# Kernel tuning notes

Measured on AMD Instinct MI355X. Metric: run time of the kernel, lower is better.

Reference implementation:

```python
import jax, jax.numpy as jnp
import numpy as np

# Model hyperparameters (from init_kwargs)
B, C, H, W = 4, 3, 224, 224
P = 16            # patch size
E = 768           # embed_dim
NH = 12           # num_heads
DH = E // NH      # head dim
L = 2             # num_layers
DFF = 4 * E
OUT = 1000
NP_ = (H // P) * (W // P)   # 196 patches
ALPHA, BETA, GAMMA = 0.5, 0.5, 1.0
EPS = 1e-8
LN_EPS = 1e-5


def _layernorm(x, w, b):
    mu = x.mean(-1, keepdims=True)
    var = ((x - mu) ** 2).mean(-1, keepdims=True)
    return (x - mu) * jax.lax.rsqrt(var + LN_EPS) * w + b


def _tversky_attn(x, ln_w, ln_b, w_qkv, b_qkv, w_o, b_o):
    # x: [B,S,E]
    h = _layernorm(x, ln_w, ln_b)
    qkv = h @ w_qkv + b_qkv                       # [B,S,3E]
    q, k, v = jnp.split(qkv, 3, axis=-1)
    def heads(t):
        return t.reshape(t.shape[0], t.shape[1], NH, DH).transpose(0, 2, 1, 3)  # [B,NH,S,DH]
    q, k, v = heads(q), heads(k), heads(v)
    # Tversky similarity on non-negative feature memberships
    qp = jax.nn.relu(q)
    kp = jax.nn.relu(k)
    qs = qp.sum(-1)                               # [B,NH,S]
    ks = kp.sum(-1)                               # [B,NH,S]
    # pairwise L1: sum_d |q_i - k_j|   (dominant intermediate [B,NH,S,S,DH])
    l1 = jnp.abs(qp[:, :, :, None, :] - kp[:, :, None, :, :]).sum(-1)  # [B,NH,S,S]
    qsum = qs[:, :, :, None]
    ksum = ks[:, :, None, :]
    inter = 0.5 * (qsum + ksum - l1)              # sum min(q,k)
    a_minus_b = 0.5 * (l1 + qsum - ksum)          # sum relu(q-k)
    b_minus_a = 0.5 * (l1 - qsum + ksum)          # sum relu(k-q)
    scores = GAMMA * inter / (inter + ALPHA * a_minus_b + BETA * b_minus_a + EPS)
    attn = jax.nn.softmax(scores, axis=-1)        # [B,NH,S,S]
    o = jnp.einsum('bhij,bhjd->bhid', attn, v)    # [B,NH,S,DH]
    o = o.transpose(0, 2, 1, 3).reshape(x.shape[0], x.shape[1], E)
    return o @ w_o + b_o


def _forward(x, conv_w, conv_b, pos_embed, cls_token,
             ln1_w, ln1_b, attn_w, attn_b, proj_w, proj_b,
             ln2_w, ln2_b, fc1_w, fc1_b, fc2_w, fc2_b,
             lnf_w, lnf_b, head_w, head_b):
    b = x.shape[0]
    # patch embed: stride==kernel conv == non-overlapping patch projection
    xp = x.reshape(b, C, H // P, P, W // P, P)
    tok = jnp.einsum('bchpwq,ecpq->bhwe', xp, conv_w).reshape(b, NP_, E) + conv_b
    tok = tok + pos_embed                         # [B,196,E]
    cls = jnp.broadcast_to(cls_token, (b, 1, E))
    h = jnp.concatenate([cls, tok], axis=1)       # [B,197,E]
    for i in range(L):
        h = h + _tversky_attn(h, ln1_w[i], ln1_b[i], attn_w[i], attn_b[i], proj_w[i], proj_b[i])
        m = _layernorm(h, ln2_w[i], ln2_b[i])
        m = jax.nn.gelu(m @ fc1_w[i] + fc1_b[i])
        h = h + m @ fc2_w[i] + fc2_b[i]
    h = _layernorm(h, lnf_w, lnf_b)
    return h[:, 0] @ head_w + head_b              # [B,OUT]


def setup_inputs() -> dict:
    key = jax.random.key(0)
    ks = jax.random.split(key, 24)
    n = lambda k, shp, s=0.02: jax.random.normal(k, shp, dtype=jnp.float32) * s
    return {
        'x': jax.random.normal(ks[0], (B, C, H, W), dtype=jnp.float32),
        'conv_w': n(ks[1], (E, C, P, P)),
        'conv_b': jnp.zeros((E,), jnp.float32),
        'pos_embed': n(ks[2], (1, NP_, E)),
        'cls_token': n(ks[3], (1, 1, E)),
        'ln1_w': jnp.ones((L, E), jnp.float32),
        'ln1_b': jnp.zeros((L, E), jnp.float32),
        'attn_w': n(ks[4], (L, E, 3 * E)),
        'attn_b': jnp.zeros((L, 3 * E), jnp.float32),
        'proj_w': n(ks[5], (L, E, E)),
        'proj_b': jnp.zeros((L, E), jnp.float32),
        'ln2_w': jnp.ones((L, E), jnp.float32),
        'ln2_b': jnp.zeros((L, E), jnp.float32),
        'fc1_w': n(ks[6], (L, E, DFF)),
        'fc1_b': jnp.zeros((L, DFF), jnp.float32),
        'fc2_w': n(ks[7], (L, DFF, E)),
        'fc2_b': jnp.zeros((L, E), jnp.float32),
        'lnf_w': jnp.ones((E,), jnp.float32),
        'lnf_b': jnp.zeros((E,), jnp.float32),
        'head_w': n(ks[8], (E, OUT)),
        'head_b': jnp.zeros((OUT,), jnp.float32),
    }


def reference(x, conv_w, conv_b, pos_embed, cls_token,
              ln1_w, ln1_b, attn_w, attn_b, proj_w, proj_b,
              ln2_w, ln2_b, fc1_w, fc1_b, fc2_w, fc2_b,
              lnf_w, lnf_b, head_w, head_b):
    return _forward(x, conv_w, conv_b, pos_embed, cls_token,
                    ln1_w, ln1_b, attn_w, attn_b, proj_w, proj_b,
                    ln2_w, ln2_b, fc1_w, fc1_b, fc2_w, fc2_b,
                    lnf_w, lnf_b, head_w, head_b)
```

## Files before the change

### kernel.cpp

```cpp
#include <hip/hip_runtime.h>
#include <hip/hip_bf16.h>
#include <math.h>

#define B_  4
#define E_  768
#define NH_ 12
#define DH_ 64
#define DFF_ 3072
#define OUT_ 1000
#define S_  197
#define ROWS_ 788
#define QH_P 12608
#define KGP  16384

typedef __bf16 bf16x8_t __attribute__((ext_vector_type(8)));
typedef float f32x4_t __attribute__((ext_vector_type(4)));
typedef _Float16 f16x2_t __attribute__((ext_vector_type(2)));

#define HAS_FDOT2 __has_builtin(__builtin_amdgcn_fdot2)

__device__ __forceinline__ float gelu_f(float x) {
    float x3 = x * x * x;
    return 0.5f * x * (1.0f + tanhf(0.7978845608028654f * (x + 0.044715f * x3)));
}
__device__ __forceinline__ ushort f_to_bf16bits(float f) {
    __hip_bfloat16 b = __float2bfloat16(f);
    return *(ushort*)&b;
}
__device__ __forceinline__ ushort f_to_f16bits(float f) {
    _Float16 h = (_Float16)f;
    return __builtin_bit_cast(ushort, h);
}
__device__ __forceinline__ f16x2_t u2h(uint u) { return __builtin_bit_cast(f16x2_t, u); }
__device__ __forceinline__ f16x2_t min2(f16x2_t a, f16x2_t b) {
    return __builtin_elementwise_min(a, b);
}

#define WT_CONV   0
#define WT_LBASE  589824
#define WT_LSTRIDE 7077888
#define WT_QKV    0
#define WT_PROJ   1769472
#define WT_FC1    2359296
#define WT_FC2    4718592
__global__ __launch_bounds__(256) void prep_all_kernel(const float* __restrict__ x,
                                                       __hip_bfloat16* __restrict__ aim,
                                                       const float* __restrict__ attn_w,
                                                       const float* __restrict__ proj_w,
                                                       const float* __restrict__ fc1_w,
                                                       const float* __restrict__ fc2_w,
                                                       const float* __restrict__ conv_w,
                                                       __hip_bfloat16* __restrict__ wt) {
    int bid = blockIdx.x;
    if (bid < 588) {
        int id = bid * 256 + threadIdx.x;
        int row = id / 192, k4 = (id - row * 192) * 4;
        int b = row / 196, pr = row - b * 196;
        int hp = pr / 14, wp = pr - hp * 14;
        int c = k4 >> 8, rem = k4 & 255, p = rem >> 4, q = rem & 15;
        float4 v = *(const float4*)&x[(((size_t)(b * 3 + c) * 224) + hp * 16 + p) * 224 + wp * 16 + q];
        ushort4 o = make_ushort4(f_to_bf16bits(v.x), f_to_bf16bits(v.y), f_to_bf16bits(v.z), f_to_bf16bits(v.w));
        *(ushort4*)((ushort*)aim + (size_t)row * 768 + k4) = o;
        return;
    }
    int id = bid - 588;
    if (id < 3456) {
        int l = id / 1728, r = id - l * 1728;
        const float* src;
        __hip_bfloat16* dst;
        int K, N, tile;
        size_t lbase = WT_LBASE + (size_t)l * WT_LSTRIDE;
        if (r < 432)       { src = attn_w + (size_t)l * E_ * 3 * E_; dst = wt + lbase + WT_QKV;  K = E_;   N = 3 * E_; tile = r; }
        else if (r < 576)  { src = proj_w + (size_t)l * E_ * E_;     dst = wt + lbase + WT_PROJ; K = E_;   N = E_;     tile = r - 432; }
        else if (r < 1152) { src = fc1_w + (size_t)l * E_ * DFF_;    dst = wt + lbase + WT_FC1;  K = E_;   N = DFF_;   tile = r - 576; }
        else               { src = fc2_w + (size_t)l * DFF_ * E_;    dst = wt + lbase + WT_FC2;  K = DFF_; N = E_;     tile = r - 1152; }
        int ntn = N >> 6;
        int kb = (tile / ntn) * 64, nb = (tile % ntn) * 64;
        int kq = (threadIdx.x & 15) * 4, nq = (threadIdx.x >> 4) * 4;
        const float* s0 = src + (size_t)(kb + kq) * N + nb + nq;
        float4 v0 = *(const float4*)(s0);
        float4 v1 = *(const float4*)(s0 + N);
        float4 v2 = *(const float4*)(s0 + 2 * N);
        float4 v3 = *(const float4*)(s0 + 3 * N);
        __hip_bfloat16* d0 = dst + (size_t)(nb + nq) * K + kb + kq;
        *(ushort4*)(d0)         = make_ushort4(f_to_bf16bits(v0.x), f_to_bf16bits(v1.x), f_to_bf16bits(v2.x), f_to_bf16bits(v3.x));
        *(ushort4*)(d0 + K)     = make_ushort4(f_to_bf16bits(v0.y), f_to_bf16bits(v1.y), f_to_bf16bits(v2.y), f_to_bf16bits(v3.y));
        *(ushort4*)(d0 + 2 * K) = make_ushort4(f_to_bf16bits(v0.z), f_to_bf16bits(v1.z), f_to_bf16bits(v2.z), f_to_bf16bits(v3.z));
        *(ushort4*)(d0 + 3 * K) = make_ushort4(f_to_bf16bits(v0.w), f_to_bf16bits(v1.w), f_to_bf16bits(v2.w), f_to_bf16bits(v3.w));
        return;
    }
    {
        int off = ((id - 3456) * 256 + threadIdx.x) * 4;
        float4 v = *(const float4*)&conv_w[off];
        ushort4 o = make_ushort4(f_to_bf16bits(v.x), f_to_bf16bits(v.y), f_to_bf16bits(v.z), f_to_bf16bits(v.w));
        *(ushort4*)((ushort*)wt + WT_CONV + off) = o;
    }
}

#define BK 64
#define AP 72
__global__ __launch_bounds__(256) void gemm_mfma_kernel(const __hip_bfloat16* __restrict__ A,
                                                        const __hip_bfloat16* __restrict__ WT,
                                                        const float* __restrict__ bias,
                                                        const float* __restrict__ res,
                                                        float* __restrict__ Cf,
                                                        __hip_bfloat16* __restrict__ Cb,
                                                        float* __restrict__ partbase,
                                                        int M, int N, int K, int act, int KS,
                                                        int res_pitch, int pn, int nofs) {
    __shared__ __align__(16) ushort Asb[2][64 * AP];
    __shared__ __align__(16) ushort Bsb[2][64 * AP];
    const int tid = threadIdx.x;
    const int wave = tid >> 6, lane = tid & 63;
    const int quad = lane >> 4, l15 = lane & 15;
    const int wm = wave >> 1, wn = wave & 1;
    const int m0 = blockIdx.y * 64, n0 = blockIdx.x * 64;

    const int Kc   = K / KS;
    const int kbeg = blockIdx.z * Kc;
    const int n_it = Kc / BK;

    f32x4_t acc[2][2] = {};

    const int c0r = tid >> 3,         c0o = (tid & 7) * 8;
    const int c1r = (tid + 256) >> 3, c1o = c0o;

    uint4 pa0, pa1, pb0, pb1;
    auto load_tile = [&](int kk) {
        pa0 = make_uint4(0, 0, 0, 0);
        pa1 = pa0;
        int gm = m0 + c0r;
        if (gm < M) pa0 = *(const uint4*)&A[(size_t)gm * K + kk + c0o];
        gm = m0 + c1r;
        if (gm < M) pa1 = *(const uint4*)&A[(size_t)gm * K + kk + c1o];
        pb0 = *(const uint4*)&WT[(size_t)(n0 + c0r) * K + kk + c0o];
        pb1 = *(const uint4*)&WT[(size_t)(n0 + c1r) * K + kk + c1o];
    };
    auto store_tile = [&](int buf) {
        *(uint4*)&Asb[buf][c0r * AP + c0o] = pa0;
        *(uint4*)&Asb[buf][c1r * AP + c1o] = pa1;
        *(uint4*)&Bsb[buf][c0r * AP + c0o] = pb0;
        *(uint4*)&Bsb[buf][c1r * AP + c1o] = pb1;
    };

    load_tile(kbeg);
    store_tile(0);
    if (n_it > 1) load_tile(kbeg + BK);
    __syncthreads();

    for (int it = 0; it < n_it; ++it) {
        const int cur = it & 1, nxt = cur ^ 1;
        if (it + 1 < n_it) {
            store_tile(nxt);
            if (it + 2 < n_it) load_tile(kbeg + (it + 2) * BK);
        }
        const ushort* As = Asb[cur];
        const ushort* Bs = Bsb[cur];
#pragma unroll
        for (int ks = 0; ks < BK; ks += 32) {
            bf16x8_t a0 = *(const bf16x8_t*)&As[(32 * wm + l15) * AP + ks + 8 * quad];
            bf16x8_t a1 = *(const bf16x8_t*)&As[(32 * wm + 16 + l15) * AP + ks + 8 * quad];
            bf16x8_t b0 = *(const bf16x8_t*)&Bs[(32 * wn + l15) * AP + ks + 8 * quad];
            bf16x8_t b1 = *(const bf16x8_t*)&Bs[(32 * wn + 16 + l15) * AP + ks + 8 * quad];
            acc[0][0] = __builtin_amdgcn_mfma_f32_16x16x32_bf16(a0, b0, acc[0][0], 0, 0, 0);
            acc[0][1] = __builtin_amdgcn_mfma_f32_16x16x32_bf16(a0, b1, acc[0][1], 0, 0, 0);
            acc[1][0] = __builtin_amdgcn_mfma_f32_16x16x32_bf16(a1, b0, acc[1][0], 0, 0, 0);
            acc[1][1] = __builtin_amdgcn_mfma_f32_16x16x32_bf16(a1, b1, acc[1][1], 0, 0, 0);
        }
        __syncthreads();
    }

    if (partbase) {
        float* P = partbase + (size_t)blockIdx.z * M * pn;
#pragma unroll
        for (int mi = 0; mi < 2; ++mi)
#pragma unroll
            for (int ni = 0; ni < 2; ++ni) {
                int gn = n0 + 32 * wn + 16 * ni + l15;
#pragma unroll
                for (int r = 0; r < 4; ++r) {
                    int gm = m0 + 32 * wm + 16 * mi + quad * 4 + r;
                    if (gm < M) P[(size_t)gm * pn + nofs + gn] = acc[mi][ni][r];
                }
            }
        return;
    }

#pragma unroll
    for (int mi = 0; mi < 2; ++mi)
#pragma unroll
        for (int ni = 0; ni < 2; ++ni) {
            int gn = n0 + 32 * wn + 16 * ni + l15;
#pragma unroll
            for (int r = 0; r < 4; ++r) {
                int gm = m0 + 32 * wm + 16 * mi + quad * 4 + r;
                if (gm < M) {
                    float v = acc[mi][ni][r] + bias[gn];
                    if (act == 1) v = gelu_f(v);
                    if (res) v += res[(size_t)gm * res_pitch + gn];
                    if (Cf) Cf[(size_t)gm * N + gn] = v;
                    else    Cb[(size_t)gm * N + gn] = __float2bfloat16(v);
                }
            }
        }
}

__global__ __launch_bounds__(256) void embed_ln_kernel(const float* __restrict__ p0,
                                                       const float* __restrict__ p1,
                                                       const float* __restrict__ cb,
                                                       const float* __restrict__ pe,
                                                       const float* __restrict__ ct,
                                                       const float* __restrict__ lw,
                                                       const float* __restrict__ lb,
                                                       float* __restrict__ h,
                                                       __hip_bfloat16* __restrict__ y) {
    int row = blockIdx.x, tid = threadIdx.x;
    int b = row / S_, s = row - b * S_;
    float v[3];
#pragma unroll
    for (int c = 0; c < 3; ++c) {
        int e = tid + c * 256;
        float t;
        if (s == 0) t = ct[e];
        else {
            int pr = s - 1;
            size_t gi = (size_t)(b * 196 + pr) * E_ + e;
            t = p0[gi] + p1[gi] + cb[e] + pe[(size_t)pr * E_ + e];
        }
        h[(size_t)row * E_ + e] = t;
        v[c] = t;
    }
    float sm = v[0] + v[1] + v[2];
    float sq = v[0] * v[0] + v[1] * v[1] + v[2] * v[2];
#pragma unroll
    for (int m = 1; m < 64; m <<= 1) {
        sm += __shfl_xor(sm, m, 64);
        sq += __shfl_xor(sq, m, 64);
    }
    __shared__ float ss[4], sqs[4];
    int wave = tid >> 6, lane = tid & 63;
    if (lane == 0) { ss[wave] = sm; sqs[wave] = sq; }
    __syncthreads();
    sm = ss[0] + ss[1] + ss[2] + ss[3];
    sq = sqs[0] + sqs[1] + sqs[2] + sqs[3];
    float mu   = sm * (1.0f / 768.0f);
    float var  = sq * (1.0f / 768.0f) - mu * mu;
    float rstd = rsqrtf(var + 1e-5f);
    __hip_bfloat16* yr = y + (size_t)row * E_;
#pragma unroll
    for (int c = 0; c < 3; ++c) {
        int e = tid + c * 256;
        yr[e] = __float2bfloat16((v[c] - mu) * rstd * lw[e] + lb[e]);
    }
}

__global__ __launch_bounds__(256) void layernorm_kernel(const float* __restrict__ x,
                                                        const float* __restrict__ w,
                                                        const float* __restrict__ b,
                                                        __hip_bfloat16* __restrict__ y) {
    int row = blockIdx.x;
    const float* xr = x + (size_t)row * E_;
    int tid = threadIdx.x;
    float v0 = xr[tid], v1 = xr[tid + 256], v2 = xr[tid + 512];
    float s  = v0 + v1 + v2;
    float sq = v0 * v0 + v1 * v1 + v2 * v2;
#pragma unroll
    for (int m = 1; m < 64; m <<= 1) {
        s  += __shfl_xor(s, m, 64);
        sq += __shfl_xor(sq, m, 64);
    }
    __shared__ float ss[4], sqs[4];
    int wave = tid >> 6, lane = tid & 63;
    if (lane == 0) { ss[wave] = s; sqs[wave] = sq; }
    __syncthreads();
    s  = ss[0] + ss[1] + ss[2] + ss[3];
    sq = sqs[0] + sqs[1] + sqs[2] + sqs[3];
    float mu   = s * (1.0f / 768.0f);
    float var  = sq * (1.0f / 768.0f) - mu * mu;
    float rstd = rsqrtf(var + 1e-5f);
    __hip_bfloat16* yr = y + (size_t)row * E_;
    yr[tid]       = __float2bfloat16((v0 - mu) * rstd * w[tid]       + b[tid]);
    yr[tid + 256] = __float2bfloat16((v1 - mu) * rstd * w[tid + 256] + b[tid + 256]);
    yr[tid + 512] = __float2bfloat16((v2 - mu) * rstd * w[tid + 512] + b[tid + 512]);
}

__global__ __launch_bounds__(256) void reduce_ln_kernel(const float* __restrict__ parts,
                                                        int np, size_t pstride,
                                                        const float* __restrict__ bias,
                                                        float* __restrict__ h,
                                                        const float* __restrict__ lw,
                                                        const float* __restrict__ lb,
                                                        __hip_bfloat16* __restrict__ y) {
    int row = blockIdx.x, tid = threadIdx.x;
    float v[3];
#pragma unroll
    for (int c = 0; c < 3; ++c) {
        int e = tid + c * 256;
        size_t gi = (size_t)row * E_ + e;
        float t = bias[e] + h[gi];
        for (int z = 0; z < np; ++z) t += parts[z * pstride + gi];
        h[gi] = t;
        v[c] = t;
    }
    float s  = v[0] + v[1] + v[2];
    float sq = v[0] * v[0] + v[1] * v[1] + v[2] * v[2];
#pragma unroll
    for (int m = 1; m < 64; m <<= 1) {
        s  += __shfl_xor(s, m, 64);
        sq += __shfl_xor(sq, m, 64);
    }
    __shared__ float ss[4], sqs[4];
    int wave = tid >> 6, lane = tid & 63;
    if (lane == 0) { ss[wave] = s; sqs[wave] = sq; }
    __syncthreads();
    s  = ss[0] + ss[1] + ss[2] + ss[3];
    sq = sqs[0] + sqs[1] + sqs[2] + sqs[3];
    float mu   = s * (1.0f / 768.0f);
    float var  = sq * (1.0f / 768.0f) - mu * mu;
    float rstd = rsqrtf(var + 1e-5f);
    __hip_bfloat16* yr = y + (size_t)row * E_;
#pragma unroll
    for (int c = 0; c < 3; ++c) {
        int e = tid + c * 256;
        yr[e] = __float2bfloat16((v[c] - mu) * rstd * lw[e] + lb[e]);
    }
}

__global__ __launch_bounds__(256) void attn_prep_kernel(const float* __restrict__ p0,
                                                        const float* __restrict__ p1,
                                                        const float* __restrict__ ab,
                                                        ushort* __restrict__ kg,
                                                        float* __restrict__ ksg,
                                                        ushort* __restrict__ qg,
                                                        ushort* __restrict__ vgt,
                                                        float* __restrict__ qsg,
                                                        int nrows,
                                                        const __hip_bfloat16* __restrict__ xin,
                                                        const float* __restrict__ wraw) {
    const int tid = threadIdx.x, lane = tid & 63, wv = tid >> 6;
    const int hh = blockIdx.x, bb = blockIdx.y, z = blockIdx.z;
    const int head = bb * NH_ + hh;
    if (z < 2) {
        const int jb = z * 128;
        float* ksrow = ksg + (size_t)head * 256;
        for (int c = 0; c < 32; ++c) {
            int j = jb + c * 4 + wv;
            float val;
            if (j < S_) {
                size_t g = ((size_t)(bb * S_ + j)) * (3 * E_) + E_ + hh * DH_ + lane;
                val = fmaxf(p0[g] + p1[g] + ab[E_ + hh * DH_ + lane], 0.f);
            } else val = -64.f;
            kg[(size_t)head * KGP + j * 64 + lane] = f_to_f16bits(val);
            float s = (j < S_) ? val : 0.f;
#pragma unroll
            for (int m = 1; m < 64; m <<= 1) s += __shfl_xor(s, m, 64);
            if (lane == 0) ksrow[j] = s;
        }
    } else if (z < 4) {
        __shared__ ushort t[64][130];
        const int jb = (z - 2) * 128;
        for (int c = 0; c < 32; ++c) {
            int idx = c * 256 + tid;
            int jl = idx >> 6, d = idx & 63;
            int j = jb + jl;
            float val = 0.f;
            if (j < S_) {
                size_t g = ((size_t)(bb * S_ + j)) * (3 * E_) + 2 * E_ + hh * DH_ + d;
                val = p0[g] + p1[g] + ab[2 * E_ + hh * DH_ + d];
            }
            t[d][jl] = f_to_bf16bits(val);
        }
        __syncthreads();
        for (int c = 0; c < 32; ++c) {
            int idx = c * 256 + tid;
            int d = idx >> 7, jl = idx & 127;
            vgt[(size_t)head * KGP + d * 256 + jb + jl] = t[d][jl];
        }
    } else {
        if (nrows == 1) {
            if (z == 5) return;
            __shared__ float sacc[4][64];
            const __hip_bfloat16* xr = xin + (size_t)(bb * S_) * E_;
            const float* wcol = wraw + hh * DH_;
            float acc = 0.f;
            const int k0 = wv * 192;
#pragma unroll 4
            for (int k = k0; k < k0 + 192; ++k)
                acc += __bfloat162float(xr[k]) * wcol[(size_t)k * (3 * E_) + lane];
            sacc[wv][lane] = acc;
            __syncthreads();
            if (tid < 64) {
                float q = sacc[0][tid] + sacc[1][tid] + sacc[2][tid] + sacc[3][tid] + ab[hh * DH_ + tid];
                q = fmaxf(q, 0.f);
                qg[(size_t)head * QH_P + tid] = f_to_f16bits(q);
                float s = q;
#pragma unroll
                for (int m = 1; m < 64; m <<= 1) s += __shfl_xor(s, m, 64);
                if (tid == 0) qsg[(size_t)head * 200] = s;
            }
            return;
        }
        const int ib = (z - 4) * 128;
        float* qsrow = qsg + (size_t)head * 200;
        for (int c = 0; c < 32; ++c) {
            int i = ib + c * 4 + wv;
            if (i >= nrows) continue;
            size_t g = ((size_t)(bb * S_ + i)) * (3 * E_) + hh * DH_ + lane;
            float val = fmaxf(p0[g] + p1[g] + ab[hh * DH_ + lane], 0.f);
            qg[(size_t)head * QH_P + i * 64 + lane] = f_to_f16bits(val);
            float s = val;
#pragma unroll
            for (int m = 1; m < 64; m <<= 1) s += __shfl_xor(s, m, 64);
            if (lane == 0) qsrow[i] = s;
        }
    }
}

__global__ __launch_bounds__(256) void tversky_attn_kernel(const ushort* __restrict__ qg,
                                                           const ushort* __restrict__ kg,
                                                           const float* __restrict__ ksg,
                                                           const ushort* __restrict__ vgt,
                                                           const float* __restrict__ qsg,
                                                           __hip_bfloat16* __restrict__ ao,
                                                           int nrows) {
    __shared__ __align__(16) ushort kf[16384];
    __shared__ __align__(16) float ks_l[256];
    __shared__ __align__(16) ushort q_l[1024];
    __shared__ __align__(16) ushort p_l[4096];
    __shared__ __align__(16) float den_l[16];

    const int tid = threadIdx.x, wv = tid >> 6, lane = tid & 63;
    const int quad = lane >> 4, l15 = lane & 15;
    const int ch = blockIdx.x, hh = blockIdx.y, bb = blockIdx.z;
    const int head = bb * NH_ + hh;

    {
        const ushort* kgh = kg + (size_t)head * KGP;
#pragma unroll
        for (int g = 0; g < 8; ++g) {
            int idx = g * 256 + tid;
            int row = idx >> 3, c = idx & 7;
            int sw = c ^ ((row >> 1) & 7);
            *(uint4*)&kf[row * 64 + sw * 8] = *(const uint4*)&kgh[idx * 8];
        }
        ks_l[tid] = ksg[(size_t)head * 256 + tid];
    }
    const int i0 = ch * 16 + wv * 4;
    if (lane < 32) {
        int r = lane >> 3, c = lane & 7;
        int i = i0 + r;
        uint4 qv = make_uint4(0, 0, 0, 0);
        if (i < nrows) qv = *(const uint4*)&qg[(size_t)head * QH_P + i * 64 + c * 8];
        *(uint4*)&q_l[wv * 256 + r * 64 + c * 8] = qv;
    }
    float qs_r[4];
#pragma unroll
    for (int r = 0; r < 4; ++r)
        qs_r[r] = (i0 + r < nrows) ? qsg[(size_t)head * 200 + i0 + r] : 0.f;
    __syncthreads();

#if HAS_FDOT2
    const f16x2_t one2 = __builtin_bit_cast(f16x2_t, 0x3C003C00u);
#endif
    float den_r[4] = {0.f, 0.f, 0.f, 0.f};
#pragma unroll
    for (int ph = 0; ph < 2; ++ph) {
        const int jb = ph * 128;
        const int r0 = (jb + 2 * lane) * 64;
        float acc0[4] = {0.f, 0.f, 0.f, 0.f};
        float acc1[4] = {0.f, 0.f, 0.f, 0.f};
#pragma unroll 1
        for (int hf = 0; hf < 2; ++hf) {
            uint4 kreg0[4], kreg1[4];
#pragma unroll
            for (int c = 0; c < 4; ++c) {
                int sw = ((hf * 4 + c) ^ (lane & 7)) * 8;
                kreg0[c] = *(const uint4*)&kf[r0 + sw];
                kreg1[c] = *(const uint4*)&kf[r0 + 64 + sw];
            }
#pragma unroll
            for (int c = 0; c < 4; ++c) {
                int cc = hf * 4 + c;
                uint k0p[4] = {kreg0[c].x, kreg0[c].y, kreg0[c].z, kreg0[c].w};
                uint k1p[4] = {kreg1[c].x, kreg1[c].y, kreg1[c].z, kreg1[c].w};
#pragma unroll
                for (int r = 0; r < 4; ++r) {
                    uint4 qu = *(const uint4*)&q_l[wv * 256 + r * 64 + cc * 8];
                    uint qp[4] = {qu.x, qu.y, qu.z, qu.w};
#if HAS_FDOT2
#pragma unroll
                    for (int p = 0; p < 4; ++p) {
                        f16x2_t qq = u2h(qp[p]);
                        acc0[r] = __builtin_amdgcn_fdot2(min2(qq, u2h(k0p[p])), one2, acc0[r], false);
                        acc1[r] = __builtin_amdgcn_fdot2(min2(qq, u2h(k1p[p])), one2, acc1[r], false);
                    }
#else
                    f16x2_t m0 = min2(u2h(qp[0]), u2h(k0p[0]));
                    f16x2_t m1 = min2(u2h(qp[0]), u2h(k1p[0]));
#pragma unroll
                    for (int p = 1; p < 4; ++p) {
                        m0 = m0 + min2(u2h(qp[p]), u2h(k0p[p]));
                        m1 = m1 + min2(u2h(qp[p]), u2h(k1p[p]));
                    }
                    acc0[r] += (float)m0[0] + (float)m0[1];
                    acc1[r] += (float)m1[0] + (float)m1[1];
#endif
                }
            }
        }
        float2 ks2 = *(const float2*)&ks_l[jb + 2 * lane];
#pragma unroll
        for (int r = 0; r < 4; ++r) {
            float s0 = qs_r[r] + ks2.x, s1 = qs_r[r] + ks2.y;
            float e0 = __expf((2.f * acc0[r]) / (s0 + 2e-8f));
            float e1 = __expf((2.f * acc1[r]) / (s1 + 2e-8f));
            float sum = e0 + e1;
#pragma unroll
            for (int m = 1; m < 64; m <<= 1) sum += __shfl_xor(sum, m, 64);
            den_r[r] += sum;
            uint pw = (uint)f_to_bf16bits(e0) | ((uint)f_to_bf16bits(e1) << 16);
            int i = wv * 4 + r;
            *(uint*)&p_l[(i * 256 + jb + 2 * lane) ^ ((i & 7) * 8)] = pw;
        }
    }
    if (lane == 0) {
#pragma unroll
        for (int r = 0; r < 4; ++r) den_l[wv * 4 + r] = den_r[r];
    }
    __syncthreads();

    const ushort* vb = vgt + (size_t)head * KGP + (size_t)(16 * wv + l15) * 256;
    f32x4_t accv = {0.f, 0.f, 0.f, 0.f};
#pragma unroll
    for (int st = 0; st < 8; ++st) {
        bf16x8_t a = *(const bf16x8_t*)&p_l[(l15 * 256 + st * 32 + quad * 8) ^ ((l15 & 7) * 8)];
        bf16x8_t b = *(const bf16x8_t*)&vb[st * 32 + quad * 8];
        accv = __builtin_amdgcn_mfma_f32_16x16x32_bf16(a, b, accv, 0, 0, 0);
    }
    float4 dv = *(const float4*)&den_l[quad * 4];
    float dar[4] = {dv.x, dv.y, dv.z, dv.w};
#pragma unroll
    for (int t = 0; t < 4; ++t) {
        int ig = ch * 16 + quad * 4 + t;
        if (ig < nrows)
            ao[((size_t)(bb * nrows + ig)) * E_ + hh * DH_ + 16 * wv + l15] =
                __float2bfloat16(accv[t] / dar[t]);
    }
}

__global__ __launch_bounds__(256) void head_ln_kernel(const float* __restrict__ hc,
                                                      const float* __restrict__ pc0,
                                                      const float* __restrict__ pc1,
                                                      const float* __restrict__ fb,
                                                      const float* __restrict__ lw,
                                                      const float* __restrict__ lb,
                                                      const float* __restrict__ hw,
                                                      const float* __restrict__ hb,
                                                      float* __restrict__ out) {
    int b = blockIdx.y;
    int tid = threadIdx.x;
    const float* xr0 = hc  + (size_t)b * E_;
    const float* pr0 = pc0 + (size_t)b * E_;
    const float* pr1 = pc1 + (size_t)b * E_;
    float v0 = xr0[tid]       + pr0[tid]       + pr1[tid]       + fb[tid];
    float v1 = xr0[tid + 256] + pr0[tid + 256] + pr1[tid + 256] + fb[tid + 256];
    float v2 = xr0[tid + 512] + pr0[tid + 512] + pr1[tid + 512] + fb[tid + 512];
    float s  = v0 + v1 + v2;
    float sq = v0 * v0 + v1 * v1 + v2 * v2;
#pragma unroll
    for (int m = 1; m < 64; m <<= 1) {
        s  += __shfl_xor(s, m, 64);
        sq += __shfl_xor(sq, m, 64);
    }
    __shared__ float ss[4], sqs[4];
    __shared__ float xr[E_];
    __shared__ float partial[4][64];
    int wave = tid >> 6, lane = tid & 63;
    if (lane == 0) { ss[wave] = s; sqs[wave] = sq; }
    __syncthreads();
    s  = ss[0] + ss[1] + ss[2] + ss[3];
    sq = sqs[0] + sqs[1] + sqs[2] + sqs[3];
    float mu   = s * (1.0f / 768.0f);
    float var  = sq * (1.0f / 768.0f) - mu * mu;
    float rstd = rsqrtf(var + 1e-5f);
    xr[tid]       = (v0 - mu) * rstd * lw[tid]       + lb[tid];
    xr[tid + 256] = (v1 - mu) * rstd * lw[tid + 256] + lb[tid + 256];
    xr[tid + 512] = (v2 - mu) * rstd * lw[tid + 512] + lb[tid + 512];
    __syncthreads();
    int nl = tid & 63, eq = tid >> 6;
    int n = blockIdx.x * 64 + nl;
    float acc = 0.f;
    if (n < OUT_) {
        int e0 = eq * 192;
        for (int e = e0; e < e0 + 192; ++e) acc += xr[e] * hw[(size_t)e * OUT_ + n];
    }
    partial[eq][nl] = acc;
    __syncthreads();
    if (eq == 0 && n < OUT_)
        out[(size_t)b * OUT_ + n] = partial[0][nl] + partial[1][nl] + partial[2][nl] + partial[3][nl] + hb[n];
}

extern "C" void kernel_launch(void* const* d_in, const int* in_sizes, int n_in,
                              void* d_out, int out_size, void* d_ws, size_t ws_size,
                              hipStream_t stream) {
    const float* x        = (const float*)d_in[0];
    const float* conv_w   = (const float*)d_in[1];
    const float* conv_b   = (const float*)d_in[2];
    const float* pos_e    = (const float*)d_in[3];
    const float* cls_t    = (const float*)d_in[4];
    const float* ln1_w    = (const float*)d_in[5];
    const float* ln1_b    = (const float*)d_in[6];
    const float* attn_w   = (const float*)d_in[7];
    const float* attn_b   = (const float*)d_in[8];
    const float* proj_w   = (const float*)d_in[9];
    const float* proj_b   = (const float*)d_in[10];
    const float* ln2_w    = (const float*)d_in[11];
    const float* ln2_b    = (const float*)d_in[12];
    const float* fc1_w    = (const float*)d_in[13];
    const float* fc1_b    = (const float*)d_in[14];
    const float* fc2_w    = (const float*)d_in[15];
    const float* fc2_b    = (const float*)d_in[16];
    const float* lnf_w    = (const float*)d_in[17];
    const float* lnf_b    = (const float*)d_in[18];
    const float* head_w   = (const float*)d_in[19];
    const float* head_b   = (const float*)d_in[20];
    float* out = (float*)d_out;

    float* h       = (float*)d_ws;
    float* part0q  = h + 605184;
    float* part1q  = part0q + 1815552;
    float* part    = part1q + 1815552;
    float* hc      = part + 3631104;
    float* partc   = hc + 3072;
    float* ksg     = partc + 6144;
    float* qsg     = ksg + 12288;
    __hip_bfloat16* lnb  = (__hip_bfloat16*)(qsg + 9600);
    __hip_bfloat16* ao   = lnb + 605184;
    __hip_bfloat16* hid  = ao + 605184;
    __hip_bfloat16* aim  = hid + 2420736;
    __hip_bfloat16* wt   = aim + 602112;
    ushort* kg  = (ushort*)(wt + 14745600);
    ushort* vgt = kg + 786432;
    ushort* qg  = vgt + 786432;
    __hip_bfloat16* lnb4 = (__hip_bfloat16*)(qg + 605184);
    __hip_bfloat16* hid4 = lnb4 + 3072;

    prep_all_kernel<<<4620, 256, 0, stream>>>(x, aim, attn_w, proj_w, fc1_w, fc2_w, conv_w, wt);
    {
        dim3 grid(E_ / 64, 13, 2);
        gemm_mfma_kernel<<<grid, 256, 0, stream>>>(aim, wt + WT_CONV, nullptr, nullptr, nullptr,
                                                   nullptr, part, 784, E_, E_, 0, 2, 0, E_, 0);
    }
    embed_ln_kernel<<<ROWS_, 256, 0, stream>>>(part, part + 602112, conv_b,
                                               pos_e, cls_t, ln1_w, ln1_b, h, lnb);

    {
        const __hip_bfloat16* wl = wt + WT_LBASE;
        {
            dim3 grid((3 * E_) / 64, 13, 2);
            gemm_mfma_kernel<<<grid, 256, 0, stream>>>(lnb, wl + WT_QKV, nullptr, nullptr,
                                                       nullptr, nullptr, part0q,
                                                       ROWS_, 3 * E_, E_, 0, 2, 0, 3 * E_, 0);
        }
        attn_prep_kernel<<<dim3(NH_, B_, 6), 256, 0, stream>>>(
            part0q, part1q, attn_b, kg, ksg, qg, vgt, qsg, S_, lnb, attn_w);
        tversky_attn_kernel<<<dim3(13, NH_, B_), 256, 0, stream>>>(
            qg, kg, ksg, vgt, qsg, ao, S_);
        {
            dim3 grid(E_ / 64, 13, 2);
            gemm_mfma_kernel<<<grid, 256, 0, stream>>>(ao, wl + WT_PROJ, nullptr, nullptr, nullptr,
                                                       nullptr, part, ROWS_, E_, E_, 0, 2, 0, E_, 0);
        }
        reduce_ln_kernel<<<ROWS_, 256, 0, stream>>>(part, 2, 605184, proj_b,
                                                    h, ln2_w, ln2_b, lnb);
        {
            dim3 grid(DFF_ / 64, 13);
            gemm_mfma_kernel<<<grid, 256, 0, stream>>>(lnb, wl + WT_FC1, fc1_b,
                                                       nullptr, nullptr, hid, nullptr,
                                                       ROWS_, DFF_, E_, 1, 1, 0, DFF_, 0);
        }
        {
            dim3 grid(E_ / 64, 13, 2);
            gemm_mfma_kernel<<<grid, 256, 0, stream>>>(hid, wl + WT_FC2, nullptr, nullptr, nullptr,
                                                       nullptr, part, ROWS_, E_, DFF_, 0, 2, 0, E_, 0);
        }
        reduce_ln_kernel<<<ROWS_, 256, 0, stream>>>(part, 2, 605184, fc2_b,
                                                    h, ln1_w + E_, ln1_b + E_, lnb);
    }

    {
        const __hip_bfloat16* wl = wt + WT_LBASE + WT_LSTRIDE;
        {
            dim3 grid(1536 / 64, 13, 2);
            gemm_mfma_kernel<<<grid, 256, 0, stream>>>(lnb, wl + WT_QKV + 768 * E_, nullptr, nullptr,
                                                       nullptr, nullptr, part0q,
                                                       ROWS_, 1536, E_, 0, 2, 0, 3 * E_, 768);
        }
        attn_prep_kernel<<<dim3(NH_, B_, 6), 256, 0, stream>>>(
            part0q, part1q, attn_b + 3 * E_, kg, ksg, qg, vgt, qsg, 1,
            lnb, attn_w + (size_t)E_ * 3 * E_);
        tversky_attn_kernel<<<dim3(1, NH_, B_), 256, 0, stream>>>(
            qg, kg, ksg, vgt, qsg, ao, 1);
        {
            dim3 grid(E_ / 64, 1, 1);
            gemm_mfma_kernel<<<grid, 256, 0, stream>>>(ao, wl + WT_PROJ, proj_b + E_, h,
                                                       hc, nullptr, nullptr,
                                                       4, E_, E_, 0, 1, S_ * E_, E_, 0);
        }
        layernorm_kernel<<<4, 256, 0, stream>>>(hc, ln2_w + E_, ln2_b + E_, lnb4);
        {
            dim3 grid(DFF_ / 64, 1, 1);
            gemm_mfma_kernel<<<grid, 256, 0, stream>>>(lnb4, wl + WT_FC1, fc1_b + DFF_,
                                                       nullptr, nullptr, hid4, nullptr,
                                                       4, DFF_, E_, 1, 1, 0, DFF_, 0);
        }
        {
            dim3 grid(E_ / 64, 1, 2);
            gemm_mfma_kernel<<<grid, 256, 0, stream>>>(hid4, wl + WT_FC2, nullptr, nullptr, nullptr,
                                                       nullptr, partc, 4, E_, DFF_, 0, 2, 0, E_, 0);
        }
    }

    {
        dim3 grid((OUT_ + 63) / 64, B_);
        head_ln_kernel<<<grid, 256, 0, stream>>>(hc, partc, partc + 3072, fc2_b + E_,
                                                 lnf_w, lnf_b, head_w, head_b, out);
    }
}
```

Measured before the change: 332.1 us.

## Fuse QKV GEMM with bias, relu, head scatter and row sums, drop split-K

Replaces the split-K QKV GEMM plus separate attn_prep kernel with one GEMM whose epilogue adds bias, applies relu, writes q/k as fp16 head-major, writes v transposed in bf16, and computes per-row q/k sums. Padding rows of K are now filled inside the attention kernel, and the padding region of the transposed V buffer is zeroed once in the prep kernel. This removes the fp32 partial-sum round trip and one launch per layer, at the cost of half the GEMM blocks (no K split) and scattered epilogue stores. The layer-2 CLS query path moves to a dedicated small kernel.

```diff
diff --git a/kernel.cpp b/kernel.cpp
--- a/kernel.cpp
+++ b/kernel.cpp
@@ -50,7 +50,8 @@
                                                        const float* __restrict__ fc1_w,
                                                        const float* __restrict__ fc2_w,
                                                        const float* __restrict__ conv_w,
-                                                       __hip_bfloat16* __restrict__ wt) {
+                                                       __hip_bfloat16* __restrict__ wt,
+                                                       ushort* __restrict__ vgt) {
     int bid = blockIdx.x;
     if (bid < 588) {
         int id = bid * 256 + threadIdx.x;
@@ -89,11 +90,18 @@
         *(ushort4*)(d0 + 3 * K) = make_ushort4(f_to_bf16bits(v0.w), f_to_bf16bits(v1.w), f_to_bf16bits(v2.w), f_to_bf16bits(v3.w));
         return;
     }
-    {
-        int off = ((id - 3456) * 256 + threadIdx.x) * 4;
+    id -= 3456;
+    if (id < 576) {
+        int off = (id * 256 + threadIdx.x) * 4;
         float4 v = *(const float4*)&conv_w[off];
         ushort4 o = make_ushort4(f_to_bf16bits(v.x), f_to_bf16bits(v.y), f_to_bf16bits(v.z), f_to_bf16bits(v.w));
         *(ushort4*)((ushort*)wt + WT_CONV + off) = o;
+        return;
+    }
+    id -= 576;
+    {
+        int off = (id * 256 + threadIdx.x) * 4;
+        *(ushort4*)&vgt[off] = make_ushort4(0, 0, 0, 0);
     }
 }
 
@@ -205,6 +213,142 @@
         }
 }
 
+__global__ __launch_bounds__(256) void gemm_qkv_kernel(const __hip_bfloat16* __restrict__ A,
+                                                       const __hip_bfloat16* __restrict__ WT,
+                                                       const float* __restrict__ ab,
+                                                       ushort* __restrict__ qg,
+                                                       float* __restrict__ qsg,
+                                                       ushort* __restrict__ kg,
+                                                       float* __restrict__ ksg,
+                                                       ushort* __restrict__ vgt,
+                                                       int ncol0) {
+    __shared__ __align__(16) ushort Asb[2][64 * AP];
+    __shared__ __align__(16) ushort Bsb[2][64 * AP];
+    __shared__ float rs[2][64];
+    const int tid = threadIdx.x;
+    const int wave = tid >> 6, lane = tid & 63;
+    const int quad = lane >> 4, l15 = lane & 15;
+    const int wm = wave >> 1, wn = wave & 1;
+    const int m0 = blockIdx.y * 64;
+    const int n0g = ncol0 + blockIdx.x * 64;
+
+    f32x4_t acc[2][2] = {};
+
+    const int c0r = tid >> 3,         c0o = (tid & 7) * 8;
+    const int c1r = (tid + 256) >> 3, c1o = c0o;
+
+    uint4 pa0, pa1, pb0, pb1;
+    auto load_tile = [&](int kk) {
+        pa0 = make_uint4(0, 0, 0, 0);
+        pa1 = pa0;
+        int gm = m0 + c0r;
+        if (gm < ROWS_) pa0 = *(const uint4*)&A[(size_t)gm * E_ + kk + c0o];
+        gm = m0 + c1r;
+        if (gm < ROWS_) pa1 = *(const uint4*)&A[(size_t)gm * E_ + kk + c1o];
+        pb0 = *(const uint4*)&WT[(size_t)(n0g + c0r) * E_ + kk + c0o];
+        pb1 = *(const uint4*)&WT[(size_t)(n0g + c1r) * E_ + kk + c1o];
+    };
+    auto store_tile = [&](int buf) {
+        *(uint4*)&Asb[buf][c0r * AP + c0o] = pa0;
+        *(uint4*)&Asb[buf][c1r * AP + c1o] = pa1;
+        *(uint4*)&Bsb[buf][c0r * AP + c0o] = pb0;
+        *(uint4*)&Bsb[buf][c1r * AP + c1o] = pb1;
+    };
+
+    load_tile(0);
+    store_tile(0);
+    load_tile(BK);
+    __syncthreads();
+
+    const int n_it = E_ / BK;
+    for (int it = 0; it < n_it; ++it) {
+        const int cur = it & 1, nxt = cur ^ 1;
+        if (it + 1 < n_it) {
+            store_tile(nxt);
+            if (it + 2 < n_it) load_tile((it + 2) * BK);
+        }
+        const ushort* As = Asb[cur];
+        const ushort* Bs = Bsb[cur];
+#pragma unroll
+        for (int ks = 0; ks < BK; ks += 32) {
+            bf16x8_t a0 = *(const bf16x8_t*)&As[(32 * wm + l15) * AP + ks + 8 * quad];
+            bf16x8_t a1 = *(const bf16x8_t*)&As[(32 * wm + 16 + l15) * AP + ks + 8 * quad];
+            bf16x8_t b0 = *(const bf16x8_t*)&Bs[(32 * wn + l15) * AP + ks + 8 * quad];
+            bf16x8_t b1 = *(const bf16x8_t*)&Bs[(32 * wn + 16 + l15) * AP + ks + 8 * quad];
+            acc[0][0] = __builtin_amdgcn_mfma_f32_16x16x32_bf16(a0, b0, acc[0][0], 0, 0, 0);
+            acc[0][1] = __builtin_amdgcn_mfma_f32_16x16x32_bf16(a0, b1, acc[0][1], 0, 0, 0);
+            acc[1][0] = __builtin_amdgcn_mfma_f32_16x16x32_bf16(a1, b0, acc[1][0], 0, 0, 0);
+            acc[1][1] = __builtin_amdgcn_mfma_f32_16x16x32_bf16(a1, b1, acc[1][1], 0, 0, 0);
+        }
+        __syncthreads();
+    }
+
+    const int region = n0g / 768;
+    const int hh = (n0g >> 6) % 12;
+    const float bias0 = ab[n0g + 32 * wn + l15];
+    const float bias1 = ab[n0g + 32 * wn + 16 + l15];
+
+    float rsum[2][4] = {};
+#pragma unroll
+    for (int mi = 0; mi < 2; ++mi)
+#pragma unroll
+        for (int ni = 0; ni < 2; ++ni) {
+            const int d = 32 * wn + 16 * ni + l15;
+#pragma unroll
+            for (int r = 0; r < 4; ++r) {
+                int gm = m0 + 32 * wm + 16 * mi + quad * 4 + r;
+                if (gm < ROWS_) {
+                    float v = acc[mi][ni][r] + (ni ? bias1 : bias0);
+                    int b = gm / S_, j = gm - b * S_;
+                    int head = b * NH_ + hh;
+                    if (region == 0) {
+                        v = fmaxf(v, 0.f);
+                        qg[(size_t)head * QH_P + j * 64 + d] = f_to_f16bits(v);
+                        rsum[mi][r] += v;
+                    } else if (region == 1) {
+                        v = fmaxf(v, 0.f);
+                        kg[(size_t)head * KGP + j * 64 + d] = f_to_f16bits(v);
+                        rsum[mi][r] += v;
+                    } else {
+                        vgt[(size_t)head * KGP + d * 256 + j] = f_to_bf16bits(v);
+                    }
+                }
+            }
+        }
+
+    if (region < 2) {
+#pragma unroll
+        for (int mi = 0; mi < 2; ++mi)
+#pragma unroll
+            for (int r = 0; r < 4; ++r) {
+                float s = rsum[mi][r];
+                s += __shfl_xor(s, 1, 64);
+                s += __shfl_xor(s, 2, 64);
+                s += __shfl_xor(s, 4, 64);
+                s += __shfl_xor(s, 8, 64);
+                rsum[mi][r] = s;
+            }
+        if (l15 == 0) {
+#pragma unroll
+            for (int mi = 0; mi < 2; ++mi)
+#pragma unroll
+                for (int r = 0; r < 4; ++r)
+                    rs[wn][32 * wm + 16 * mi + quad * 4 + r] = rsum[mi][r];
+        }
+        __syncthreads();
+        if (tid < 64) {
+            int gm = m0 + tid;
+            if (gm < ROWS_) {
+                int b = gm / S_, j = gm - b * S_;
+                int head = b * NH_ + hh;
+                float s = rs[0][tid] + rs[1][tid];
+                if (region == 0) qsg[(size_t)head * 200 + j] = s;
+                else             ksg[(size_t)head * 256 + j] = s;
+            }
+        }
+    }
+}
+
 __global__ __launch_bounds__(256) void embed_ln_kernel(const float* __restrict__ p0,
                                                        const float* __restrict__ p1,
                                                        const float* __restrict__ cb,
@@ -326,93 +470,32 @@
     }
 }
 
-__global__ __launch_bounds__(256) void attn_prep_kernel(const float* __restrict__ p0,
-                                                        const float* __restrict__ p1,
-                                                        const float* __restrict__ ab,
-                                                        ushort* __restrict__ kg,
-                                                        float* __restrict__ ksg,
-                                                        ushort* __restrict__ qg,
-                                                        ushort* __restrict__ vgt,
-                                                        float* __restrict__ qsg,
-                                                        int nrows,
-                                                        const __hip_bfloat16* __restrict__ xin,
-                                                        const float* __restrict__ wraw) {
+__global__ __launch_bounds__(256) void cls_q_kernel(const __hip_bfloat16* __restrict__ xin,
+                                                    const float* __restrict__ wraw,
+                                                    const float* __restrict__ ab,
+                                                    ushort* __restrict__ qg,
+                                                    float* __restrict__ qsg) {
     const int tid = threadIdx.x, lane = tid & 63, wv = tid >> 6;
-    const int hh = blockIdx.x, bb = blockIdx.y, z = blockIdx.z;
+    const int hh = blockIdx.x, bb = blockIdx.y;
     const int head = bb * NH_ + hh;
-    if (z < 2) {
-        const int jb = z * 128;
-        float* ksrow = ksg + (size_t)head * 256;
-        for (int c = 0; c < 32; ++c) {
-            int j = jb + c * 4 + wv;
-            float val;
-            if (j < S_) {
-                size_t g = ((size_t)(bb * S_ + j)) * (3 * E_) + E_ + hh * DH_ + lane;
-                val = fmaxf(p0[g] + p1[g] + ab[E_ + hh * DH_ + lane], 0.f);
-            } else val = -64.f;
-            kg[(size_t)head * KGP + j * 64 + lane] = f_to_f16bits(val);
-            float s = (j < S_) ? val : 0.f;
-#pragma unroll
-            for (int m = 1; m < 64; m <<= 1) s += __shfl_xor(s, m, 64);
-            if (lane == 0) ksrow[j] = s;
-        }
-    } else if (z < 4) {
-        __shared__ ushort t[64][130];
-        const int jb = (z - 2) * 128;
-        for (int c = 0; c < 32; ++c) {
-            int idx = c * 256 + tid;
-            int jl = idx >> 6, d = idx & 63;
-            int j = jb + jl;
-            float val = 0.f;
-            if (j < S_) {
-                size_t g = ((size_t)(bb * S_ + j)) * (3 * E_) + 2 * E_ + hh * DH_ + d;
-                val = p0[g] + p1[g] + ab[2 * E_ + hh * DH_ + d];
-            }
-            t[d][jl] = f_to_bf16bits(val);
-        }
-        __syncthreads();
-        for (int c = 0; c < 32; ++c) {
-            int idx = c * 256 + tid;
-            int d = idx >> 7, jl = idx & 127;
-            vgt[(size_t)head * KGP + d * 256 + jb + jl] = t[d][jl];
-        }
-    } else {
-        if (nrows == 1) {
-            if (z == 5) return;
-            __shared__ float sacc[4][64];
-            const __hip_bfloat16* xr = xin + (size_t)(bb * S_) * E_;
-            const float* wcol = wraw + hh * DH_;
-            float acc = 0.f;
-            const int k0 = wv * 192;
+    __shared__ float sacc[4][64];
+    const __hip_bfloat16* xr = xin + (size_t)(bb * S_) * E_;
+    const float* wcol = wraw + hh * DH_;
+    float acc = 0.f;
+    const int k0 = wv * 192;
 #pragma unroll 4
-            for (int k = k0; k < k0 + 192; ++k)
-                acc += __bfloat162float(xr[k]) * wcol[(size_t)k * (3 * E_) + lane];
-            sacc[wv][lane] = acc;
-            __syncthreads();
-            if (tid < 64) {
-                float q = sacc[0][tid] + sacc[1][tid] + sacc[2][tid] + sacc[3][tid] + ab[hh * DH_ + tid];
-                q = fmaxf(q, 0.f);
-                qg[(size_t)head * QH_P + tid] = f_to_f16bits(q);
-                float s = q;
-#pragma unroll
-                for (int m = 1; m < 64; m <<= 1) s += __shfl_xor(s, m, 64);
-                if (tid == 0) qsg[(size_t)head * 200] = s;
-            }
-            return;
-        }
-        const int ib = (z - 4) * 128;
-        float* qsrow = qsg + (size_t)head * 200;
-        for (int c = 0; c < 32; ++c) {
-            int i = ib + c * 4 + wv;
-            if (i >= nrows) continue;
-            size_t g = ((size_t)(bb * S_ + i)) * (3 * E_) + hh * DH_ + lane;
-            float val = fmaxf(p0[g] + p1[g] + ab[hh * DH_ + lane], 0.f);
-            qg[(size_t)head * QH_P + i * 64 + lane] = f_to_f16bits(val);
-            float s = val;
-#pragma unroll
-            for (int m = 1; m < 64; m <<= 1) s += __shfl_xor(s, m, 64);
-            if (lane == 0) qsrow[i] = s;
-        }
+    for (int k = k0; k < k0 + 192; ++k)
+        acc += __bfloat162float(xr[k]) * wcol[(size_t)k * (3 * E_) + lane];
+    sacc[wv][lane] = acc;
+    __syncthreads();
+    if (tid < 64) {
+        float q = sacc[0][tid] + sacc[1][tid] + sacc[2][tid] + sacc[3][tid] + ab[hh * DH_ + tid];
+        q = fmaxf(q, 0.f);
+        qg[(size_t)head * QH_P + tid] = f_to_f16bits(q);
+        float s = q;
+#pragma unroll
+        for (int m = 1; m < 64; m <<= 1) s += __shfl_xor(s, m, 64);
+        if (tid == 0) qsg[(size_t)head * 200] = s;
     }
 }
 
@@ -441,9 +524,12 @@
             int idx = g * 256 + tid;
             int row = idx >> 3, c = idx & 7;
             int sw = c ^ ((row >> 1) & 7);
-            *(uint4*)&kf[row * 64 + sw * 8] = *(const uint4*)&kgh[idx * 8];
-        }
-        ks_l[tid] = ksg[(size_t)head * 256 + tid];
+            uint4 kv;
+            if (row < S_) kv = *(const uint4*)&kgh[idx * 8];
+            else kv = make_uint4(0xD400D400u, 0xD400D400u, 0xD400D400u, 0xD400D400u);
+            *(uint4*)&kf[row * 64 + sw * 8] = kv;
+        }
+        ks_l[tid] = (tid < S_) ? ksg[(size_t)head * 256 + tid] : 0.f;
     }
     const int i0 = ch * 16 + wv * 4;
     if (lane < 32) {
@@ -645,7 +731,7 @@
     __hip_bfloat16* lnb4 = (__hip_bfloat16*)(qg + 605184);
     __hip_bfloat16* hid4 = lnb4 + 3072;
 
-    prep_all_kernel<<<4620, 256, 0, stream>>>(x, aim, attn_w, proj_w, fc1_w, fc2_w, conv_w, wt);
+    prep_all_kernel<<<5388, 256, 0, stream>>>(x, aim, attn_w, proj_w, fc1_w, fc2_w, conv_w, wt, vgt);
     {
         dim3 grid(E_ / 64, 13, 2);
         gemm_mfma_kernel<<<grid, 256, 0, stream>>>(aim, wt + WT_CONV, nullptr, nullptr, nullptr,
@@ -657,13 +743,10 @@
     {
         const __hip_bfloat16* wl = wt + WT_LBASE;
         {
-            dim3 grid((3 * E_) / 64, 13, 2);
-            gemm_mfma_kernel<<<grid, 256, 0, stream>>>(lnb, wl + WT_QKV, nullptr, nullptr,
-                                                       nullptr, nullptr, part0q,
-                                                       ROWS_, 3 * E_, E_, 0, 2, 0, 3 * E_, 0);
-        }
-        attn_prep_kernel<<<dim3(NH_, B_, 6), 256, 0, stream>>>(
-            part0q, part1q, attn_b, kg, ksg, qg, vgt, qsg, S_, lnb, attn_w);
+            dim3 grid(36, 13);
+            gemm_qkv_kernel<<<grid, 256, 0, stream>>>(lnb, wl + WT_QKV, attn_b,
+                                                      qg, qsg, kg, ksg, vgt, 0);
+        }
         tversky_attn_kernel<<<dim3(13, NH_, B_), 256, 0, stream>>>(
             qg, kg, ksg, vgt, qsg, ao, S_);
         {
@@ -691,14 +774,12 @@
     {
         const __hip_bfloat16* wl = wt + WT_LBASE + WT_LSTRIDE;
         {
-            dim3 grid(1536 / 64, 13, 2);
-            gemm_mfma_kernel<<<grid, 256, 0, stream>>>(lnb, wl + WT_QKV + 768 * E_, nullptr, nullptr,
-                                                       nullptr, nullptr, part0q,
-                                                       ROWS_, 1536, E_, 0, 2, 0, 3 * E_, 768);
-        }
-        attn_prep_kernel<<<dim3(NH_, B_, 6), 256, 0, stream>>>(
-            part0q, part1q, attn_b + 3 * E_, kg, ksg, qg, vgt, qsg, 1,
-            lnb, attn_w + (size_t)E_ * 3 * E_);
+            dim3 grid(24, 13);
+            gemm_qkv_kernel<<<grid, 256, 0, stream>>>(lnb, wl + WT_QKV, attn_b + 3 * E_,
+                                                      qg, qsg, kg, ksg, vgt, 768);
+        }
+        cls_q_kernel<<<dim3(NH_, B_), 256, 0, stream>>>(
+            lnb, attn_w + (size_t)E_ * 3 * E_, attn_b + 3 * E_, qg, qsg);
         tversky_attn_kernel<<<dim3(1, NH_, B_), 256, 0, stream>>>(
             qg, kg, ksg, vgt, qsg, ao, 1);
         {
```

Result: faster. 317.9 us (-4.3%).
